# Kernel tuning notes

Measured on AMD Instinct MI355X. Metric: run time of the kernel, lower is better.

The kernel has to match this reference:

```python
import jax, jax.numpy as jnp
import numpy as np

TAU = 2.0
V_TH = 1.0


def setup_inputs() -> dict:
    key = jax.random.key(0)
    k1, k2, k3 = jax.random.split(key, 3)
    T, B, H = 128, 64, 1024
    x = jax.random.normal(k1, (T, B, H), dtype=jnp.float32)
    # nn.Linear(H, H, bias=False) weights, shape [out, in]
    W1 = jax.random.normal(k2, (H, H), dtype=jnp.float32) / np.sqrt(H)
    W2 = jax.random.normal(k3, (H, H), dtype=jnp.float32) / np.sqrt(H)
    return {"x": x, "W1": W1, "W2": W2}


def _lif_scan(x_proj):
    # x_proj: [T, B, H]; membrane v starts at 0.
    def step(v, xt):
        h = v + (xt - v) / TAU          # leaky integrate
        s = (h >= V_TH).astype(h.dtype)  # hard-threshold spike
        v_new = h * (1.0 - s)            # soft reset (to 0 on spike)
        return v_new, s

    v0 = jnp.zeros(x_proj.shape[1:], dtype=x_proj.dtype)
    _, spikes = jax.lax.scan(step, v0, x_proj)
    return spikes  # [T, B, H]


def reference(x, W1, W2):
    # fc1 applied per timestep == one batched GEMM over [T*B, H]
    x_proj = jnp.einsum('tbh,oh->tbo', x, W1)
    spike = _lif_scan(x_proj)
    out = jnp.einsum('tbh,oh->tbo', spike, W2)
    return out
```

## Files before the change

kernel.cpp:

```cpp
#include <hip/hip_runtime.h>
#include <hip/hip_bf16.h>
#include <stdint.h>

#define TT 128
#define BB 64
#define HH 1024
#define MM (TT * BB)
#define NLANE (BB * HH)
#define DELTA 3.0e-5
#define CAPL 32768
#define LO_SCALE 4096.0f
#define F16_ONE 0x3C00

typedef __attribute__((ext_vector_type(8))) _Float16 f16x8;
typedef __attribute__((ext_vector_type(4))) float f32x4;

#define GLOAD16(g, l)                                                        \
    __builtin_amdgcn_global_load_lds(                                        \
        (const __attribute__((address_space(1))) unsigned int*)(g),          \
        (__attribute__((address_space(3))) unsigned int*)(l), 16, 0, 0)

static __device__ __forceinline__ unsigned short f16_bits(float f) {
    _Float16 h = (_Float16)f;
    return *reinterpret_cast<unsigned short*>(&h);
}

__global__ __launch_bounds__(256) void split2_kernel(const float* __restrict__ src,
                                                     unsigned short* __restrict__ hi,
                                                     unsigned short* __restrict__ lo,
                                                     int n4) {
    const int i = blockIdx.x * 256 + threadIdx.x;
    if (i >= n4) return;
    float4 x = reinterpret_cast<const float4*>(src)[i];
    float v[4] = {x.x, x.y, x.z, x.w};
    unsigned short hb[4], lb[4];
#pragma unroll
    for (int c = 0; c < 4; c++) {
        _Float16 hh = (_Float16)v[c];
        hb[c] = *reinterpret_cast<unsigned short*>(&hh);
        lb[c] = f16_bits((v[c] - (float)hh) * LO_SCALE);
    }
    reinterpret_cast<ushort4*>(hi)[i] = make_ushort4(hb[0], hb[1], hb[2], hb[3]);
    reinterpret_cast<ushort4*>(lo)[i] = make_ushort4(lb[0], lb[1], lb[2], lb[3]);
}

__global__ __launch_bounds__(256) void cast_f16(const float* __restrict__ src,
                                                unsigned short* __restrict__ dst,
                                                int n) {
    const int i = blockIdx.x * 256 + threadIdx.x;
    if (i < n) dst[i] = f16_bits(src[i]);
}

__global__ __launch_bounds__(256) void gemm1_mfma(const unsigned short* __restrict__ Ah,
                                                  const unsigned short* __restrict__ Al,
                                                  const unsigned short* __restrict__ Bh,
                                                  const unsigned short* __restrict__ Bl,
                                                  float* __restrict__ C) {
    __shared__ short AsH[128 * 32];
    __shared__ short AsL[128 * 32];
    __shared__ short BsH[128 * 32];
    __shared__ short BsL[128 * 32];

    const int tid = threadIdx.x;
    const int lane = tid & 63;
    const int wave = tid >> 6;
    const int m0 = blockIdx.x * 128;
    const int n0 = blockIdx.y * 128;
    const int wm = (wave >> 1) * 64;
    const int wn = (wave & 1) * 64;

    const int rsel = lane & 15;
    const int part = lane >> 4;

    int adrA[4], adrB[4];
#pragma unroll
    for (int i = 0; i < 4; i++) {
        const int ra = wm + i * 16 + rsel;
        const int rb = wn + i * 16 + rsel;
        adrA[i] = ra * 32 + (part ^ ((ra >> 1) & 3)) * 8;
        adrB[i] = rb * 32 + (part ^ ((rb >> 1) & 3)) * 8;
    }

    f32x4 acc1[4][4] = {};
    f32x4 acc2[4][4] = {};

    for (int k0 = 0; k0 < HH; k0 += 32) {
#pragma unroll
        for (int p = 0; p < 2; p++) {
            const int c = tid + p * 256;
            const int cb = wave * 64 + p * 256;
            const int row = c >> 2;
            const int pslot = c & 3;
            const int pdata = pslot ^ ((row >> 1) & 3);
            const size_t goA = (size_t)(m0 + row) * HH + k0 + pdata * 8;
            const size_t goB = (size_t)(n0 + row) * HH + k0 + pdata * 8;
            GLOAD16(&Ah[goA], &AsH[cb * 8]);
            GLOAD16(&Al[goA], &AsL[cb * 8]);
            GLOAD16(&Bh[goB], &BsH[cb * 8]);
            GLOAD16(&Bl[goB], &BsL[cb * 8]);
        }
        __syncthreads();

        f16x8 aH[4], aL[4], bH[4], bL[4];
#pragma unroll
        for (int mi = 0; mi < 4; mi++) {
            aH[mi] = *reinterpret_cast<f16x8*>(&AsH[adrA[mi]]);
            aL[mi] = *reinterpret_cast<f16x8*>(&AsL[adrA[mi]]);
        }
#pragma unroll
        for (int ni = 0; ni < 4; ni++) {
            bH[ni] = *reinterpret_cast<f16x8*>(&BsH[adrB[ni]]);
            bL[ni] = *reinterpret_cast<f16x8*>(&BsL[adrB[ni]]);
        }

#pragma unroll
        for (int mi = 0; mi < 4; mi++)
#pragma unroll
            for (int ni = 0; ni < 4; ni++) {
                acc1[mi][ni] = __builtin_amdgcn_mfma_f32_16x16x32_f16(aH[mi], bH[ni], acc1[mi][ni], 0, 0, 0);
                acc2[mi][ni] = __builtin_amdgcn_mfma_f32_16x16x32_f16(aH[mi], bL[ni], acc2[mi][ni], 0, 0, 0);
                acc2[mi][ni] = __builtin_amdgcn_mfma_f32_16x16x32_f16(aL[mi], bH[ni], acc2[mi][ni], 0, 0, 0);
            }

        __syncthreads();
    }

    const int col = lane & 15;
    const int quad = lane >> 4;
    const float inv = 1.0f / LO_SCALE;
#pragma unroll
    for (int mi = 0; mi < 4; mi++)
#pragma unroll
        for (int ni = 0; ni < 4; ni++) {
            const int m = m0 + wm + mi * 16 + quad * 4;
            const int n = n0 + wn + ni * 16 + col;
            float* dst = &C[(size_t)m * HH + n];
#pragma unroll
            for (int r = 0; r < 4; r++)
                dst[(size_t)r * HH] = fmaf(acc2[mi][ni][r], inv, acc1[mi][ni][r]);
        }
}

__global__ __launch_bounds__(256) void lif_scan_flag(const float* __restrict__ xp,
                                                     unsigned short* __restrict__ sp,
                                                     int* __restrict__ count,
                                                     int* __restrict__ list) {
    const int idx = blockIdx.x * 256 + threadIdx.x;
    double v = 0.0;
    bool flg = false;
#pragma unroll 4
    for (int t = 0; t < TT; t++) {
        const double x = (double)xp[(size_t)t * NLANE + idx];
        const double h = v + (x - v) * 0.5;
        const bool s = (h >= 1.0);
        flg |= (fabs(h - 1.0) < DELTA);
        v = s ? 0.0 : h;
        sp[(size_t)t * NLANE + idx] = s ? (unsigned short)F16_ONE : (unsigned short)0;
    }
    if (flg) {
        const int i = atomicAdd(count, 1);
        list[i] = idx;
    }
}

__global__ __launch_bounds__(256) void recompute_dots(const float* __restrict__ X,
                                                      const float* __restrict__ W1,
                                                      const int* __restrict__ count,
                                                      const int* __restrict__ list,
                                                      double* __restrict__ hraw) {
    const int cnt = *count;
    const int lim = (cnt < CAPL ? cnt : CAPL);
    const long ntask = (long)lim * TT;
    const int ln = threadIdx.x & 63;
    const long wid = (long)blockIdx.x * 4 + (threadIdx.x >> 6);
    const long nwaves = (long)gridDim.x * 4;

    for (long task = wid; task < ntask; task += nwaves) {
        const int li = (int)(task >> 7);
        const int t = (int)(task & (TT - 1));
        const int lane = list[li];
        const int b = lane >> 10;
        const int h = lane & (HH - 1);
        const float4* x4 = reinterpret_cast<const float4*>(X + (size_t)(t * BB + b) * HH);
        const float4* w4 = reinterpret_cast<const float4*>(W1 + (size_t)h * HH);

        double s0 = 0.0, s1 = 0.0, s2 = 0.0, s3 = 0.0;
#pragma unroll
        for (int i = 0; i < 4; i++) {
            const float4 xa = x4[ln + i * 64];
            const float4 wa = w4[ln + i * 64];
            s0 = fma((double)xa.x, (double)wa.x, s0);
            s1 = fma((double)xa.y, (double)wa.y, s1);
            s2 = fma((double)xa.z, (double)wa.z, s2);
            s3 = fma((double)xa.w, (double)wa.w, s3);
        }
        double s = (s0 + s1) + (s2 + s3);
#pragma unroll
        for (int off = 32; off >= 1; off >>= 1)
            s += __shfl_down(s, off);
        if (ln == 0) hraw[task] = s;
    }
}

__global__ __launch_bounds__(256) void rescan_lanes(const float* __restrict__ X,
                                                    const float* __restrict__ W1,
                                                    const int* __restrict__ count,
                                                    const int* __restrict__ list,
                                                    const double* __restrict__ hraw,
                                                    unsigned short* __restrict__ sp) {
    const int li = blockIdx.x * 256 + threadIdx.x;
    const int cnt = *count;
    if (li >= cnt) return;
    const int lane = list[li];

    double v = 0.0;
    if (li < CAPL) {
        const double* hb = hraw + (size_t)li * TT;
        for (int t = 0; t < TT; t++) {
            const double h = v + (hb[t] - v) * 0.5;
            const bool s = (h >= 1.0);
            v = s ? 0.0 : h;
            sp[(size_t)t * NLANE + lane] = s ? (unsigned short)F16_ONE : (unsigned short)0;
        }
    } else {
        const int b = lane >> 10;
        const int h = lane & (HH - 1);
        const float* wrow = W1 + (size_t)h * HH;
        for (int t = 0; t < TT; t++) {
            const float* xrow = X + (size_t)(t * BB + b) * HH;
            double d = 0.0;
            for (int k = 0; k < HH; k++)
                d = fma((double)xrow[k], (double)wrow[k], d);
            const double hh = v + (d - v) * 0.5;
            const bool s = (hh >= 1.0);
            v = s ? 0.0 : hh;
            sp[(size_t)t * NLANE + lane] = s ? (unsigned short)F16_ONE : (unsigned short)0;
        }
    }
}

__global__ __launch_bounds__(256) void gemm2_mfma(const unsigned short* __restrict__ S,
                                                  const unsigned short* __restrict__ W,
                                                  float* __restrict__ O) {
    __shared__ short As[128 * 32];
    __shared__ short Bs[128 * 32];

    const int tid = threadIdx.x;
    const int lane = tid & 63;
    const int wave = tid >> 6;
    const int m0 = blockIdx.x * 128;
    const int n0 = blockIdx.y * 128;
    const int wm = (wave >> 1) * 64;
    const int wn = (wave & 1) * 64;

    const int rsel = lane & 15;
    const int part = lane >> 4;

    int adrA[4], adrB[4];
#pragma unroll
    for (int i = 0; i < 4; i++) {
        const int ra = wm + i * 16 + rsel;
        const int rb = wn + i * 16 + rsel;
        adrA[i] = ra * 32 + (part ^ ((ra >> 1) & 3)) * 8;
        adrB[i] = rb * 32 + (part ^ ((rb >> 1) & 3)) * 8;
    }

    f32x4 acc[4][4] = {};

    for (int k0 = 0; k0 < HH; k0 += 32) {
#pragma unroll
        for (int p = 0; p < 2; p++) {
            const int c = tid + p * 256;
            const int cb = wave * 64 + p * 256;
            const int row = c >> 2;
            const int pslot = c & 3;
            const int pdata = pslot ^ ((row >> 1) & 3);
            GLOAD16(&S[(size_t)(m0 + row) * HH + k0 + pdata * 8], &As[cb * 8]);
            GLOAD16(&W[(size_t)(n0 + row) * HH + k0 + pdata * 8], &Bs[cb * 8]);
        }
        __syncthreads();

        f16x8 a[4], b[4];
#pragma unroll
        for (int mi = 0; mi < 4; mi++)
            a[mi] = *reinterpret_cast<f16x8*>(&As[adrA[mi]]);
#pragma unroll
        for (int ni = 0; ni < 4; ni++)
            b[ni] = *reinterpret_cast<f16x8*>(&Bs[adrB[ni]]);

#pragma unroll
        for (int mi = 0; mi < 4; mi++)
#pragma unroll
            for (int ni = 0; ni < 4; ni++)
                acc[mi][ni] = __builtin_amdgcn_mfma_f32_16x16x32_f16(
                    a[mi], b[ni], acc[mi][ni], 0, 0, 0);

        __syncthreads();
    }

    const int col = lane & 15;
    const int quad = lane >> 4;
#pragma unroll
    for (int mi = 0; mi < 4; mi++)
#pragma unroll
        for (int ni = 0; ni < 4; ni++) {
            const int m = m0 + wm + mi * 16 + quad * 4;
            const int n = n0 + wn + ni * 16 + col;
            float* dst = &O[(size_t)m * HH + n];
#pragma unroll
            for (int r = 0; r < 4; r++)
                dst[(size_t)r * HH] = acc[mi][ni][r];
        }
}

extern "C" void kernel_launch(void* const* d_in, const int* in_sizes, int n_in,
                              void* d_out, int out_size, void* d_ws, size_t ws_size,
                              hipStream_t stream) {
    const float* x  = (const float*)d_in[0];
    const float* W1 = (const float*)d_in[1];
    const float* W2 = (const float*)d_in[2];
    float* out = (float*)d_out;

    char* ws = (char*)d_ws;
    const size_t szX = (size_t)MM * HH;
    const size_t szW = (size_t)HH * HH;

    unsigned short* Xhi  = (unsigned short*)ws;
    unsigned short* Xlo  = Xhi + szX;
    unsigned short* W1hi = Xlo + szX;
    unsigned short* W1lo = W1hi + szW;
    unsigned short* w2h  = W1lo + szW;
    int*            list = (int*)(w2h + szW);
    int*            cnt  = list + NLANE;
    float*          xp   = (float*)(((uintptr_t)(cnt + 64) + 255) & ~(uintptr_t)255);
    unsigned short* sp   = Xhi;
    double*         hraw = (double*)xp;

    hipMemsetAsync(cnt, 0, sizeof(int), stream);

    split2_kernel<<<(int)(szX / 4 / 256), 256, 0, stream>>>(x, Xhi, Xlo, (int)(szX / 4));
    split2_kernel<<<(int)(szW / 4 / 256), 256, 0, stream>>>(W1, W1hi, W1lo, (int)(szW / 4));
    cast_f16<<<(int)((szW + 255) / 256), 256, 0, stream>>>(W2, w2h, (int)szW);

    dim3 g1(MM / 128, HH / 128);
    gemm1_mfma<<<g1, 256, 0, stream>>>(Xhi, Xlo, W1hi, W1lo, xp);

    lif_scan_flag<<<NLANE / 256, 256, 0, stream>>>(xp, sp, cnt, list);

    recompute_dots<<<2048, 256, 0, stream>>>(x, W1, cnt, list, hraw);
    rescan_lanes<<<NLANE / 256, 256, 0, stream>>>(x, W1, cnt, list, hraw, sp);

    dim3 g2(MM / 128, HH / 128);
    gemm2_mfma<<<g2, 256, 0, stream>>>(sp, w2h, out);
}
```

Before: 258.5 us.

## Fuse prep kernels and recompute/rescan, merge split-GEMM accumulators

Replaces the three preprocessing launches and the memset with one fused prep kernel that picks its source by block index and zeroes the counter. Merges the flagged-lane dot-product recompute and rescan into one kernel that keeps per-timestep sums in shared memory, which drops the hraw buffer and the capacity split. In gemm1 the hi/lo correction is folded into a single accumulator each k-step, freeing registers at the cost of extra FMAs. The fused recompute rescans serially on one thread per lane, which may be slow if many lanes are flagged.

```diff
diff --git a/kernel.cpp b/kernel.cpp
--- a/kernel.cpp
+++ b/kernel.cpp
@@ -8,8 +8,8 @@
 #define MM (TT * BB)
 #define NLANE (BB * HH)
 #define DELTA 3.0e-5
-#define CAPL 32768
 #define LO_SCALE 4096.0f
+#define INV_LO (1.0f / 4096.0f)
 #define F16_ONE 0x3C00
 
 typedef __attribute__((ext_vector_type(8))) _Float16 f16x8;
@@ -25,30 +25,45 @@
     return *reinterpret_cast<unsigned short*>(&h);
 }
 
-__global__ __launch_bounds__(256) void split2_kernel(const float* __restrict__ src,
-                                                     unsigned short* __restrict__ hi,
-                                                     unsigned short* __restrict__ lo,
-                                                     int n4) {
-    const int i = blockIdx.x * 256 + threadIdx.x;
-    if (i >= n4) return;
-    float4 x = reinterpret_cast<const float4*>(src)[i];
-    float v[4] = {x.x, x.y, x.z, x.w};
+__global__ __launch_bounds__(256) void prep_fused(const float* __restrict__ x,
+                                                  const float* __restrict__ W1,
+                                                  const float* __restrict__ W2,
+                                                  unsigned short* __restrict__ Xhi,
+                                                  unsigned short* __restrict__ Xlo,
+                                                  unsigned short* __restrict__ W1hi,
+                                                  unsigned short* __restrict__ W1lo,
+                                                  unsigned short* __restrict__ w2h,
+                                                  int* __restrict__ cnt) {
+    const int bid = blockIdx.x;
+    if (bid == 0 && threadIdx.x == 0) *cnt = 0;
+
+    const float* src;
+    unsigned short *hi, *lo;
+    int i;
+    bool split;
+    if (bid < 8192) {
+        i = bid * 256 + threadIdx.x;
+        src = x; hi = Xhi; lo = Xlo; split = true;
+    } else if (bid < 9216) {
+        i = (bid - 8192) * 256 + threadIdx.x;
+        src = W1; hi = W1hi; lo = W1lo; split = true;
+    } else {
+        i = (bid - 9216) * 256 + threadIdx.x;
+        src = W2; hi = w2h; lo = nullptr; split = false;
+    }
+
+    float4 v4 = reinterpret_cast<const float4*>(src)[i];
+    float v[4] = {v4.x, v4.y, v4.z, v4.w};
     unsigned short hb[4], lb[4];
 #pragma unroll
     for (int c = 0; c < 4; c++) {
         _Float16 hh = (_Float16)v[c];
         hb[c] = *reinterpret_cast<unsigned short*>(&hh);
-        lb[c] = f16_bits((v[c] - (float)hh) * LO_SCALE);
+        if (split) lb[c] = f16_bits((v[c] - (float)hh) * LO_SCALE);
     }
     reinterpret_cast<ushort4*>(hi)[i] = make_ushort4(hb[0], hb[1], hb[2], hb[3]);
-    reinterpret_cast<ushort4*>(lo)[i] = make_ushort4(lb[0], lb[1], lb[2], lb[3]);
-}
-
-__global__ __launch_bounds__(256) void cast_f16(const float* __restrict__ src,
-                                                unsigned short* __restrict__ dst,
-                                                int n) {
-    const int i = blockIdx.x * 256 + threadIdx.x;
-    if (i < n) dst[i] = f16_bits(src[i]);
+    if (split)
+        reinterpret_cast<ushort4*>(lo)[i] = make_ushort4(lb[0], lb[1], lb[2], lb[3]);
 }
 
 __global__ __launch_bounds__(256) void gemm1_mfma(const unsigned short* __restrict__ Ah,
@@ -81,8 +96,8 @@
         adrB[i] = rb * 32 + (part ^ ((rb >> 1) & 3)) * 8;
     }
 
-    f32x4 acc1[4][4] = {};
-    f32x4 acc2[4][4] = {};
+    f32x4 acc[4][4] = {};
+    const f32x4 zero = {0.0f, 0.0f, 0.0f, 0.0f};
 
     for (int k0 = 0; k0 < HH; k0 += 32) {
 #pragma unroll
@@ -116,10 +131,19 @@
 #pragma unroll
         for (int mi = 0; mi < 4; mi++)
 #pragma unroll
+            for (int ni = 0; ni < 4; ni++)
+                acc[mi][ni] = __builtin_amdgcn_mfma_f32_16x16x32_f16(
+                    aH[mi], bH[ni], acc[mi][ni], 0, 0, 0);
+
+#pragma unroll
+        for (int mi = 0; mi < 4; mi++)
+#pragma unroll
             for (int ni = 0; ni < 4; ni++) {
-                acc1[mi][ni] = __builtin_amdgcn_mfma_f32_16x16x32_f16(aH[mi], bH[ni], acc1[mi][ni], 0, 0, 0);
-                acc2[mi][ni] = __builtin_amdgcn_mfma_f32_16x16x32_f16(aH[mi], bL[ni], acc2[mi][ni], 0, 0, 0);
-                acc2[mi][ni] = __builtin_amdgcn_mfma_f32_16x16x32_f16(aL[mi], bH[ni], acc2[mi][ni], 0, 0, 0);
+                f32x4 t = __builtin_amdgcn_mfma_f32_16x16x32_f16(aH[mi], bL[ni], zero, 0, 0, 0);
+                t = __builtin_amdgcn_mfma_f32_16x16x32_f16(aL[mi], bH[ni], t, 0, 0, 0);
+#pragma unroll
+                for (int r = 0; r < 4; r++)
+                    acc[mi][ni][r] = fmaf(t[r], INV_LO, acc[mi][ni][r]);
             }
 
         __syncthreads();
@@ -127,7 +151,6 @@
 
     const int col = lane & 15;
     const int quad = lane >> 4;
-    const float inv = 1.0f / LO_SCALE;
 #pragma unroll
     for (int mi = 0; mi < 4; mi++)
 #pragma unroll
@@ -137,7 +160,7 @@
             float* dst = &C[(size_t)m * HH + n];
 #pragma unroll
             for (int r = 0; r < 4; r++)
-                dst[(size_t)r * HH] = fmaf(acc2[mi][ni][r], inv, acc1[mi][ni][r]);
+                dst[(size_t)r * HH] = acc[mi][ni][r];
         }
 }
 
@@ -163,79 +186,52 @@
     }
 }
 
-__global__ __launch_bounds__(256) void recompute_dots(const float* __restrict__ X,
-                                                      const float* __restrict__ W1,
-                                                      const int* __restrict__ count,
-                                                      const int* __restrict__ list,
-                                                      double* __restrict__ hraw) {
+__global__ __launch_bounds__(256) void recompute_fused(const float* __restrict__ X,
+                                                       const float* __restrict__ W1,
+                                                       const int* __restrict__ count,
+                                                       const int* __restrict__ list,
+                                                       unsigned short* __restrict__ sp) {
+    __shared__ double hbuf[TT];
     const int cnt = *count;
-    const int lim = (cnt < CAPL ? cnt : CAPL);
-    const long ntask = (long)lim * TT;
+    const int wv = threadIdx.x >> 6;
     const int ln = threadIdx.x & 63;
-    const long wid = (long)blockIdx.x * 4 + (threadIdx.x >> 6);
-    const long nwaves = (long)gridDim.x * 4;
-
-    for (long task = wid; task < ntask; task += nwaves) {
-        const int li = (int)(task >> 7);
-        const int t = (int)(task & (TT - 1));
+
+    for (int li = blockIdx.x; li < cnt; li += gridDim.x) {
         const int lane = list[li];
         const int b = lane >> 10;
         const int h = lane & (HH - 1);
-        const float4* x4 = reinterpret_cast<const float4*>(X + (size_t)(t * BB + b) * HH);
         const float4* w4 = reinterpret_cast<const float4*>(W1 + (size_t)h * HH);
 
-        double s0 = 0.0, s1 = 0.0, s2 = 0.0, s3 = 0.0;
-#pragma unroll
-        for (int i = 0; i < 4; i++) {
-            const float4 xa = x4[ln + i * 64];
-            const float4 wa = w4[ln + i * 64];
-            s0 = fma((double)xa.x, (double)wa.x, s0);
-            s1 = fma((double)xa.y, (double)wa.y, s1);
-            s2 = fma((double)xa.z, (double)wa.z, s2);
-            s3 = fma((double)xa.w, (double)wa.w, s3);
-        }
-        double s = (s0 + s1) + (s2 + s3);
-#pragma unroll
-        for (int off = 32; off >= 1; off >>= 1)
-            s += __shfl_down(s, off);
-        if (ln == 0) hraw[task] = s;
-    }
-}
-
-__global__ __launch_bounds__(256) void rescan_lanes(const float* __restrict__ X,
-                                                    const float* __restrict__ W1,
-                                                    const int* __restrict__ count,
-                                                    const int* __restrict__ list,
-                                                    const double* __restrict__ hraw,
-                                                    unsigned short* __restrict__ sp) {
-    const int li = blockIdx.x * 256 + threadIdx.x;
-    const int cnt = *count;
-    if (li >= cnt) return;
-    const int lane = list[li];
-
-    double v = 0.0;
-    if (li < CAPL) {
-        const double* hb = hraw + (size_t)li * TT;
-        for (int t = 0; t < TT; t++) {
-            const double h = v + (hb[t] - v) * 0.5;
-            const bool s = (h >= 1.0);
-            v = s ? 0.0 : h;
-            sp[(size_t)t * NLANE + lane] = s ? (unsigned short)F16_ONE : (unsigned short)0;
-        }
-    } else {
-        const int b = lane >> 10;
-        const int h = lane & (HH - 1);
-        const float* wrow = W1 + (size_t)h * HH;
-        for (int t = 0; t < TT; t++) {
-            const float* xrow = X + (size_t)(t * BB + b) * HH;
-            double d = 0.0;
-            for (int k = 0; k < HH; k++)
-                d = fma((double)xrow[k], (double)wrow[k], d);
-            const double hh = v + (d - v) * 0.5;
-            const bool s = (hh >= 1.0);
-            v = s ? 0.0 : hh;
-            sp[(size_t)t * NLANE + lane] = s ? (unsigned short)F16_ONE : (unsigned short)0;
-        }
+        for (int t = wv; t < TT; t += 4) {
+            const float4* x4 = reinterpret_cast<const float4*>(X + (size_t)(t * BB + b) * HH);
+            double s0 = 0.0, s1 = 0.0, s2 = 0.0, s3 = 0.0;
+#pragma unroll
+            for (int i = 0; i < 4; i++) {
+                const float4 xa = x4[ln + i * 64];
+                const float4 wa = w4[ln + i * 64];
+                s0 = fma((double)xa.x, (double)wa.x, s0);
+                s1 = fma((double)xa.y, (double)wa.y, s1);
+                s2 = fma((double)xa.z, (double)wa.z, s2);
+                s3 = fma((double)xa.w, (double)wa.w, s3);
+            }
+            double s = (s0 + s1) + (s2 + s3);
+#pragma unroll
+            for (int off = 32; off >= 1; off >>= 1)
+                s += __shfl_down(s, off);
+            if (ln == 0) hbuf[t] = s;
+        }
+        __syncthreads();
+
+        if (threadIdx.x == 0) {
+            double v = 0.0;
+            for (int t = 0; t < TT; t++) {
+                const double hh = v + (hbuf[t] - v) * 0.5;
+                const bool s = (hh >= 1.0);
+                v = s ? 0.0 : hh;
+                sp[(size_t)t * NLANE + lane] = s ? (unsigned short)F16_ONE : (unsigned short)0;
+            }
+        }
+        __syncthreads();
     }
 }
 
@@ -334,21 +330,15 @@
     int*            cnt  = list + NLANE;
     float*          xp   = (float*)(((uintptr_t)(cnt + 64) + 255) & ~(uintptr_t)255);
     unsigned short* sp   = Xhi;
-    double*         hraw = (double*)xp;
-
-    hipMemsetAsync(cnt, 0, sizeof(int), stream);
-
-    split2_kernel<<<(int)(szX / 4 / 256), 256, 0, stream>>>(x, Xhi, Xlo, (int)(szX / 4));
-    split2_kernel<<<(int)(szW / 4 / 256), 256, 0, stream>>>(W1, W1hi, W1lo, (int)(szW / 4));
-    cast_f16<<<(int)((szW + 255) / 256), 256, 0, stream>>>(W2, w2h, (int)szW);
+
+    prep_fused<<<10240, 256, 0, stream>>>(x, W1, W2, Xhi, Xlo, W1hi, W1lo, w2h, cnt);
 
     dim3 g1(MM / 128, HH / 128);
     gemm1_mfma<<<g1, 256, 0, stream>>>(Xhi, Xlo, W1hi, W1lo, xp);
 
     lif_scan_flag<<<NLANE / 256, 256, 0, stream>>>(xp, sp, cnt, list);
 
-    recompute_dots<<<2048, 256, 0, stream>>>(x, W1, cnt, list, hraw);
-    rescan_lanes<<<NLANE / 256, 256, 0, stream>>>(x, W1, cnt, list, hraw, sp);
+    recompute_fused<<<1024, 256, 0, stream>>>(x, W1, cnt, list, sp);
 
     dim3 g2(MM / 128, HH / 128);
     gemm2_mfma<<<g2, 256, 0, stream>>>(sp, w2h, out);
```

New measurement: 231.2 us. -10.6%, faster.
